# Performance work log

Hardware: AMD Instinct MI355X
Metric: run time of the kernel (lower is better)

The kernel has to match this reference:

```python
import jax, jax.numpy as jnp
import numpy as np

B, C, T, V, F, NCLS = 2, 4, 128, 67, 64, 100


def setup_inputs() -> dict:
    key = jax.random.key(0)
    ks = jax.random.split(key, 20)
    s = 0.1
    return {
        "joint_matrix": jax.random.normal(ks[0], (B, C, T, V), jnp.float32),
        "vel_matrix": jax.random.normal(ks[1], (B, C, T, V), jnp.float32),
        # 1x1 convs stored as [out_ch, in_ch] matrices (equivalent math)
        "vc1_w": jax.random.normal(ks[2], (1, C), jnp.float32) * s,
        "vc1_b": jax.random.normal(ks[3], (1,), jnp.float32) * s,
        "vc2_w": jax.random.normal(ks[4], (1, 1), jnp.float32) * s,
        "vc2_b": jax.random.normal(ks[5], (1,), jnp.float32) * s,
        "sc1_w": jax.random.normal(ks[6], (1, C), jnp.float32) * s,
        "sc1_b": jax.random.normal(ks[7], (1,), jnp.float32) * s,
        "sc2_w": jax.random.normal(ks[8], (1, 1), jnp.float32) * s,
        "sc2_b": jax.random.normal(ks[9], (1,), jnp.float32) * s,
        # Linear(1, F, bias=False) weights, flattened to [F]
        "w_theta": jax.random.normal(ks[10], (F,), jnp.float32) * s,
        "w_void": jax.random.normal(ks[11], (F,), jnp.float32) * s,
        "w_g": jax.random.normal(ks[12], (F,), jnp.float32) * s,
        "convh_w": jax.random.normal(ks[13], (C, F), jnp.float32) * s,
        "convh_b": jax.random.normal(ks[14], (C,), jnp.float32) * s,
        "lin_w": jax.random.normal(ks[15], (NCLS, C), jnp.float32) * s,
        "lin_b": jax.random.normal(ks[16], (NCLS,), jnp.float32) * s,
    }


def _conv1x1(x, w, b):
    # x: [B, Cin, T, V], w: [Cout, Cin]
    return jnp.einsum('bchw,oc->bohw', x, w) + b[None, :, None, None]


def reference(joint_matrix, vel_matrix, vc1_w, vc1_b, vc2_w, vc2_b,
              sc1_w, sc1_b, sc2_w, sc2_b, w_theta, w_void, w_g,
              convh_w, convh_b, lin_w, lin_b):
    Vel = jax.nn.relu(_conv1x1(_conv1x1(vel_matrix, vc1_w, vc1_b), vc2_w, vc2_b))
    I = jax.nn.relu(_conv1x1(_conv1x1(joint_matrix, sc1_w, sc1_b), sc2_w, sc2_b))
    Z = Vel + I  # [B, 1, T, V]
    b, _, t, v = Z.shape
    f = w_theta.shape[0]
    Zt = jnp.transpose(Z, (0, 3, 2, 1))  # [B, V, T, 1]
    theta = (Zt * w_theta).reshape(b, v * t, f)      # [B, VT, F]
    # NOTE: original does a RAW reshape of [B,V,T,F] -> [B,F,T*V] (not a transpose)
    void = (Zt * w_void).reshape(b, f, t * v)        # [B, F, TV]
    g = (Zt * w_g).reshape(b, v * t, f)              # [B, VT, F]
    scores = jax.nn.relu(jnp.matmul(theta, void))    # [B, VT, VT]
    att = jnp.matmul(scores, g)                      # [B, VT, F]
    att = jnp.transpose(att.reshape(b, v, t, f), (0, 3, 2, 1))  # [B, F, T, V]
    att = _conv1x1(att, convh_w, convh_b) + Z        # broadcast residual -> [B, C, T, V]
    pooled = att.mean(axis=(2, 3))                   # [B, C]
    logits = pooled @ lin_w.T + lin_b                # [B, NCLS]
    return jax.nn.softmax(logits, axis=1)
```

## Files before the change

### kernel.cpp

```cpp
#include <hip/hip_runtime.h>

#define BB 2
#define CC 4
#define TT 128
#define VV 67
#define FF 64
#define NCLS 100
#define TV 8576
#define QQ 134

#define ZIDX(p) ((p) + ((p) >> 7))
#define ZLDS (TV + VV)

__global__ __launch_bounds__(1024) void ar_fused(
    const float* __restrict__ joint, const float* __restrict__ vel,
    const float* __restrict__ vc1_w, const float* __restrict__ vc1_b,
    const float* __restrict__ vc2_w, const float* __restrict__ vc2_b,
    const float* __restrict__ sc1_w, const float* __restrict__ sc1_b,
    const float* __restrict__ sc2_w, const float* __restrict__ sc2_b,
    const float* __restrict__ w_theta, const float* __restrict__ w_void,
    const float* __restrict__ w_g,
    const float* __restrict__ convh_w, const float* __restrict__ convh_b,
    const float* __restrict__ lin_w, const float* __restrict__ lin_b,
    float* __restrict__ out)
{
    const int b = blockIdx.x;
    const int tid = threadIdx.x;

    __shared__ float zs[ZLDS];
    __shared__ float wth[FF], wvd[FF];
    __shared__ float A[QQ];
    __shared__ float redS[16], redZ[16];
    __shared__ float Sv, Zm;
    __shared__ float pooled[CC];
    __shared__ float logits[NCLS], evals[NCLS];
    __shared__ float smax, sinv;

    if (tid < FF) { wth[tid] = w_theta[tid]; wvd[tid] = w_void[tid]; }

    const float v1w0 = vc1_w[0], v1w1 = vc1_w[1], v1w2 = vc1_w[2], v1w3 = vc1_w[3];
    const float s1w0 = sc1_w[0], s1w1 = sc1_w[1], s1w2 = sc1_w[2], s1w3 = sc1_w[3];
    const float v1b = vc1_b[0], v2w = vc2_w[0], v2b = vc2_b[0];
    const float s1b = sc1_b[0], s2w = sc2_w[0], s2b = sc2_b[0];

    const float4* velb = (const float4*)(vel + (size_t)b * CC * TV);
    const float4* jntb = (const float4*)(joint + (size_t)b * CC * TV);
    const int P4 = TV / 4;

    float zacc = 0.0f;
    for (int i = tid; i < P4; i += 1024) {
        float4 vA = velb[i];            float4 jA = jntb[i];
        float4 vB = velb[i + P4];       float4 jB = jntb[i + P4];
        float4 vC = velb[i + 2 * P4];   float4 jC = jntb[i + 2 * P4];
        float4 vD = velb[i + 3 * P4];   float4 jD = jntb[i + 3 * P4];

        float zv[4];
        {
            float vs, js;
            vs = v1b + vA.x * v1w0 + vB.x * v1w1 + vC.x * v1w2 + vD.x * v1w3;
            js = s1b + jA.x * s1w0 + jB.x * s1w1 + jC.x * s1w2 + jD.x * s1w3;
            zv[0] = fmaxf(v2w * vs + v2b, 0.f) + fmaxf(s2w * js + s2b, 0.f);
            vs = v1b + vA.y * v1w0 + vB.y * v1w1 + vC.y * v1w2 + vD.y * v1w3;
            js = s1b + jA.y * s1w0 + jB.y * s1w1 + jC.y * s1w2 + jD.y * s1w3;
            zv[1] = fmaxf(v2w * vs + v2b, 0.f) + fmaxf(s2w * js + s2b, 0.f);
            vs = v1b + vA.z * v1w0 + vB.z * v1w1 + vC.z * v1w2 + vD.z * v1w3;
            js = s1b + jA.z * s1w0 + jB.z * s1w1 + jC.z * s1w2 + jD.z * s1w3;
            zv[2] = fmaxf(v2w * vs + v2b, 0.f) + fmaxf(s2w * js + s2b, 0.f);
            vs = v1b + vA.w * v1w0 + vB.w * v1w1 + vC.w * v1w2 + vD.w * v1w3;
            js = s1b + jA.w * s1w0 + jB.w * s1w1 + jC.w * s1w2 + jD.w * s1w3;
            zv[3] = fmaxf(v2w * vs + v2b, 0.f) + fmaxf(s2w * js + s2b, 0.f);
        }

        int r = 4 * i;
        int t = r / VV, v = r - t * VV;
        #pragma unroll
        for (int k = 0; k < 4; ++k) {
            int p = (v << 7) + t;
            zs[ZIDX(p)] = zv[k];
            zacc += zv[k];
            if (++v == VV) { v = 0; ++t; }
        }
    }
    __syncthreads();

    if (tid < QQ) {
        float acc = 0.0f;
        #pragma unroll
        for (int f = 0; f < FF; ++f) {
            int p = f * QQ + tid;
            acc += wth[f] * zs[ZIDX(p)];
        }
        A[tid] = acc;
    }
    __syncthreads();

    float sS = 0.0f;
    for (int j = tid; j < TV; j += 1024) {
        float u = wvd[j & 63] * A[j >> 6];
        sS += fmaxf(u, 0.0f) * zs[ZIDX(j)];
    }
    #pragma unroll
    for (int off = 32; off > 0; off >>= 1) {
        sS += __shfl_down(sS, off);
        zacc += __shfl_down(zacc, off);
    }
    if ((tid & 63) == 0) { redS[tid >> 6] = sS; redZ[tid >> 6] = zacc; }
    __syncthreads();
    if (tid == 0) {
        float aS = 0.f, aZ = 0.f;
        #pragma unroll
        for (int w = 0; w < 16; ++w) { aS += redS[w]; aZ += redZ[w]; }
        Sv = aS;
        Zm = aZ / (float)TV;
    }
    __syncthreads();

    if (tid < CC) {
        float gw = 0.f;
        #pragma unroll
        for (int f = 0; f < FF; ++f) gw += convh_w[tid * FF + f] * w_g[f];
        pooled[tid] = Zm * (Sv * gw + 1.0f) + convh_b[tid];
    }
    __syncthreads();
    if (tid < NCLS) {
        float lg = lin_b[tid];
        #pragma unroll
        for (int c = 0; c < CC; ++c) lg += lin_w[tid * CC + c] * pooled[c];
        logits[tid] = lg;
    }
    __syncthreads();
    if (tid == 0) {
        float m = -1e30f;
        for (int n = 0; n < NCLS; ++n) m = fmaxf(m, logits[n]);
        smax = m;
    }
    __syncthreads();
    if (tid < NCLS) evals[tid] = expf(logits[tid] - smax);
    __syncthreads();
    if (tid == 0) {
        float s = 0.f;
        for (int n = 0; n < NCLS; ++n) s += evals[n];
        sinv = 1.0f / s;
    }
    __syncthreads();
    if (tid < NCLS) out[b * NCLS + tid] = evals[tid] * sinv;
}

extern "C" void kernel_launch(void* const* d_in, const int* in_sizes, int n_in,
                              void* d_out, int out_size, void* d_ws, size_t ws_size,
                              hipStream_t stream) {
    const float* joint  = (const float*)d_in[0];
    const float* vel    = (const float*)d_in[1];
    const float* vc1_w  = (const float*)d_in[2];
    const float* vc1_b  = (const float*)d_in[3];
    const float* vc2_w  = (const float*)d_in[4];
    const float* vc2_b  = (const float*)d_in[5];
    const float* sc1_w  = (const float*)d_in[6];
    const float* sc1_b  = (const float*)d_in[7];
    const float* sc2_w  = (const float*)d_in[8];
    const float* sc2_b  = (const float*)d_in[9];
    const float* w_theta = (const float*)d_in[10];
    const float* w_void  = (const float*)d_in[11];
    const float* w_g     = (const float*)d_in[12];
    const float* convh_w = (const float*)d_in[13];
    const float* convh_b = (const float*)d_in[14];
    const float* lin_w   = (const float*)d_in[15];
    const float* lin_b   = (const float*)d_in[16];
    float* out = (float*)d_out;

    ar_fused<<<BB, 1024, 0, stream>>>(joint, vel, vc1_w, vc1_b, vc2_w, vc2_b,
                                      sc1_w, sc1_b, sc2_w, sc2_b,
                                      w_theta, w_void, w_g,
                                      convh_w, convh_b, lin_w, lin_b, out);
}
```

Before: 12.92 us.

## Split per-batch work across cooperative grid with LDS atomics and grid sync

New measurement: 39.15 us. 203% more time.

```diff
diff --git a/kernel.cpp b/kernel.cpp
--- a/kernel.cpp
+++ b/kernel.cpp
@@ -1,4 +1,7 @@
 #include <hip/hip_runtime.h>
+#include <hip/hip_cooperative_groups.h>
+
+namespace cg = cooperative_groups;
 
 #define BB 2
 #define CC 4
@@ -8,11 +11,19 @@
 #define NCLS 100
 #define TV 8576
 #define QQ 134
-
-#define ZIDX(p) ((p) + ((p) >> 7))
-#define ZLDS (TV + VV)
-
-__global__ __launch_bounds__(1024) void ar_fused(
+#define GB 8
+#define NTH 256
+#define P4 (TV / 4)
+#define SLOTF 408
+
+__device__ __forceinline__ float agent_load(const float* p) {
+    return __hip_atomic_load(p, __ATOMIC_RELAXED, __HIP_MEMORY_SCOPE_AGENT);
+}
+__device__ __forceinline__ void agent_store(float* p, float v) {
+    __hip_atomic_store(p, v, __ATOMIC_RELAXED, __HIP_MEMORY_SCOPE_AGENT);
+}
+
+__global__ __launch_bounds__(NTH) void ar_coop(
     const float* __restrict__ joint, const float* __restrict__ vel,
     const float* __restrict__ vc1_w, const float* __restrict__ vc1_b,
     const float* __restrict__ vc2_w, const float* __restrict__ vc2_b,
@@ -22,21 +33,32 @@
     const float* __restrict__ w_g,
     const float* __restrict__ convh_w, const float* __restrict__ convh_b,
     const float* __restrict__ lin_w, const float* __restrict__ lin_b,
-    float* __restrict__ out)
+    float* __restrict__ out, float* __restrict__ ws)
 {
-    const int b = blockIdx.x;
+    const int blk = blockIdx.x;
+    const int b = blk / GB;
+    const int g = blk % GB;
     const int tid = threadIdx.x;
-
-    __shared__ float zs[ZLDS];
-    __shared__ float wth[FF], wvd[FF];
-    __shared__ float A[QQ];
-    __shared__ float redS[16], redZ[16];
-    __shared__ float Sv, Zm;
+    const int lane = tid & 63, wave = tid >> 6;
+
+    __shared__ float Ap[QQ], Zp[QQ], Zn[QQ];
+    __shared__ float wth[FF], wvp[FF], wvn[FF];
+    __shared__ float Zs;
+    __shared__ float rs[4], rz[4];
+    __shared__ float Svv, Zmm;
     __shared__ float pooled[CC];
     __shared__ float logits[NCLS], evals[NCLS];
     __shared__ float smax, sinv;
 
-    if (tid < FF) { wth[tid] = w_theta[tid]; wvd[tid] = w_void[tid]; }
+    for (int i = tid; i < QQ; i += NTH) { Ap[i] = 0.f; Zp[i] = 0.f; Zn[i] = 0.f; }
+    if (tid == 0) Zs = 0.f;
+    if (tid < FF) {
+        float w = w_void[tid];
+        wvp[tid] = fmaxf(w, 0.f);
+        wvn[tid] = fminf(w, 0.f);
+        wth[tid] = w_theta[tid];
+    }
+    __syncthreads();
 
     const float v1w0 = vc1_w[0], v1w1 = vc1_w[1], v1w2 = vc1_w[2], v1w3 = vc1_w[3];
     const float s1w0 = sc1_w[0], s1w1 = sc1_w[1], s1w2 = sc1_w[2], s1w3 = sc1_w[3];
@@ -45,10 +67,9 @@
 
     const float4* velb = (const float4*)(vel + (size_t)b * CC * TV);
     const float4* jntb = (const float4*)(joint + (size_t)b * CC * TV);
-    const int P4 = TV / 4;
-
-    float zacc = 0.0f;
-    for (int i = tid; i < P4; i += 1024) {
+
+    float zacc = 0.f;
+    for (int i = g * NTH + tid; i < P4; i += GB * NTH) {
         float4 vA = velb[i];            float4 jA = jntb[i];
         float4 vB = velb[i + P4];       float4 jB = jntb[i + P4];
         float4 vC = velb[i + 2 * P4];   float4 jC = jntb[i + 2 * P4];
@@ -76,52 +97,67 @@
         #pragma unroll
         for (int k = 0; k < 4; ++k) {
             int p = (v << 7) + t;
-            zs[ZIDX(p)] = zv[k];
-            zacc += zv[k];
+            float zz = zv[k];
+            atomicAdd(&Ap[p % QQ], wth[p / QQ] * zz);
+            atomicAdd(&Zp[p >> 6], wvp[p & 63] * zz);
+            atomicAdd(&Zn[p >> 6], wvn[p & 63] * zz);
+            zacc += zz;
             if (++v == VV) { v = 0; ++t; }
         }
     }
-    __syncthreads();
-
+    #pragma unroll
+    for (int off = 32; off > 0; off >>= 1) zacc += __shfl_down(zacc, off);
+    if (lane == 0) atomicAdd(&Zs, zacc);
+    __syncthreads();
+
+    float* slot = ws + (size_t)blk * SLOTF;
+    for (int i = tid; i < QQ; i += NTH) {
+        agent_store(slot + i,          Ap[i]);
+        agent_store(slot + QQ + i,     Zp[i]);
+        agent_store(slot + 2 * QQ + i, Zn[i]);
+    }
+    if (tid == 0) agent_store(slot + 3 * QQ, Zs);
+
+    cg::this_grid().sync();
+
+    if (g != 0) return;
+
+    const float* base = ws + (size_t)b * GB * SLOTF;
+    float sq = 0.f, zq = 0.f;
     if (tid < QQ) {
-        float acc = 0.0f;
-        #pragma unroll
-        for (int f = 0; f < FF; ++f) {
-            int p = f * QQ + tid;
-            acc += wth[f] * zs[ZIDX(p)];
+        float a = 0.f, zp = 0.f, zn = 0.f;
+        #pragma unroll
+        for (int gg = 0; gg < GB; ++gg) {
+            const float* sl = base + gg * SLOTF;
+            a  += agent_load(sl + tid);
+            zp += agent_load(sl + QQ + tid);
+            zn += agent_load(sl + 2 * QQ + tid);
         }
-        A[tid] = acc;
-    }
-    __syncthreads();
-
-    float sS = 0.0f;
-    for (int j = tid; j < TV; j += 1024) {
-        float u = wvd[j & 63] * A[j >> 6];
-        sS += fmaxf(u, 0.0f) * zs[ZIDX(j)];
-    }
+        sq = a * (a >= 0.f ? zp : zn);
+    }
+    if (tid < GB) zq = agent_load(base + tid * SLOTF + 3 * QQ);
+
     #pragma unroll
     for (int off = 32; off > 0; off >>= 1) {
-        sS += __shfl_down(sS, off);
-        zacc += __shfl_down(zacc, off);
-    }
-    if ((tid & 63) == 0) { redS[tid >> 6] = sS; redZ[tid >> 6] = zacc; }
+        sq += __shfl_down(sq, off);
+        zq += __shfl_down(zq, off);
+    }
+    if (lane == 0) { rs[wave] = sq; rz[wave] = zq; }
     __syncthreads();
     if (tid == 0) {
-        float aS = 0.f, aZ = 0.f;
-        #pragma unroll
-        for (int w = 0; w < 16; ++w) { aS += redS[w]; aZ += redZ[w]; }
-        Sv = aS;
-        Zm = aZ / (float)TV;
-    }
-    __syncthreads();
-
-    if (tid < CC) {
-        float gw = 0.f;
-        #pragma unroll
-        for (int f = 0; f < FF; ++f) gw += convh_w[tid * FF + f] * w_g[f];
-        pooled[tid] = Zm * (Sv * gw + 1.0f) + convh_b[tid];
-    }
-    __syncthreads();
+        Svv = rs[0] + rs[1] + rs[2] + rs[3];
+        Zmm = (rz[0] + rz[1] + rz[2] + rz[3]) / (float)TV;
+    }
+    __syncthreads();
+
+    {
+        float gv = convh_w[wave * FF + lane] * w_g[lane];
+        #pragma unroll
+        for (int off = 32; off > 0; off >>= 1) gv += __shfl_down(gv, off);
+        if (lane == 0) pooled[wave] = Zmm * (Svv * gv + 1.0f) + convh_b[wave];
+    }
+    __syncthreads();
+
     if (tid < NCLS) {
         float lg = lin_b[tid];
         #pragma unroll
@@ -129,18 +165,22 @@
         logits[tid] = lg;
     }
     __syncthreads();
-    if (tid == 0) {
+    if (wave == 0) {
         float m = -1e30f;
-        for (int n = 0; n < NCLS; ++n) m = fmaxf(m, logits[n]);
-        smax = m;
+        for (int n = lane; n < NCLS; n += 64) m = fmaxf(m, logits[n]);
+        #pragma unroll
+        for (int off = 32; off > 0; off >>= 1) m = fmaxf(m, __shfl_down(m, off));
+        if (lane == 0) smax = m;
     }
     __syncthreads();
     if (tid < NCLS) evals[tid] = expf(logits[tid] - smax);
     __syncthreads();
-    if (tid == 0) {
+    if (wave == 0) {
         float s = 0.f;
-        for (int n = 0; n < NCLS; ++n) s += evals[n];
-        sinv = 1.0f / s;
+        for (int n = lane; n < NCLS; n += 64) s += evals[n];
+        #pragma unroll
+        for (int off = 32; off > 0; off >>= 1) s += __shfl_down(s, off);
+        if (lane == 0) sinv = 1.0f / s;
     }
     __syncthreads();
     if (tid < NCLS) out[b * NCLS + tid] = evals[tid] * sinv;
@@ -167,9 +207,16 @@
     const float* lin_w   = (const float*)d_in[15];
     const float* lin_b   = (const float*)d_in[16];
     float* out = (float*)d_out;
-
-    ar_fused<<<BB, 1024, 0, stream>>>(joint, vel, vc1_w, vc1_b, vc2_w, vc2_b,
-                                      sc1_w, sc1_b, sc2_w, sc2_b,
-                                      w_theta, w_void, w_g,
-                                      convh_w, convh_b, lin_w, lin_b, out);
-}
+    float* ws  = (float*)d_ws;
+
+    void* args[] = {
+        (void*)&joint, (void*)&vel,
+        (void*)&vc1_w, (void*)&vc1_b, (void*)&vc2_w, (void*)&vc2_b,
+        (void*)&sc1_w, (void*)&sc1_b, (void*)&sc2_w, (void*)&sc2_b,
+        (void*)&w_theta, (void*)&w_void, (void*)&w_g,
+        (void*)&convh_w, (void*)&convh_b, (void*)&lin_w, (void*)&lin_b,
+        (void*)&out, (void*)&ws
+    };
+    hipLaunchCooperativeKernel((const void*)ar_coop, dim3(BB * GB), dim3(NTH),
+                               args, 0, stream);
+}
```
